# Kernel optimization log

Measured on AMD Instinct MI355X. Metric: run time of the kernel, lower is better.

The kernel has to match this reference:

```python
import jax, jax.numpy as jnp
import numpy as np

N = 100000      # nodes
E = 1600000     # edges
F = 64          # num_features
C = 10          # num_classes
L = 4           # num_layers
B = 128         # graphs in batch


def setup_inputs() -> dict:
    key = jax.random.key(0)
    ks = jax.random.split(key, 8)
    x = jax.random.normal(ks[0], (N, F), dtype=jnp.float32)
    edge_index = jax.random.randint(ks[1], (2, E), 0, N, dtype=jnp.int64)
    batch = jnp.sort(jax.random.randint(ks[2], (N,), 0, B, dtype=jnp.int64))
    scale = 1.0 / jnp.sqrt(jnp.float32(F))
    W1s = jax.random.normal(ks[3], (L, F, F), dtype=jnp.float32) * scale
    W2s = jax.random.normal(ks[4], (L, F, F), dtype=jnp.float32) * scale
    fc_w = jax.random.normal(ks[5], (C, F), dtype=jnp.float32) * scale
    fc_b = jax.random.normal(ks[6], (C,), dtype=jnp.float32) * 0.01
    return {"x": x, "edge_index": edge_index, "batch": batch,
            "W1s": W1s, "W2s": W2s, "fc_w": fc_w, "fc_b": fc_b}


def reference(x, edge_index, batch, W1s, W2s, fc_w, fc_b):
    src, dst = edge_index[0], edge_index[1]
    h = x
    for l in range(L):  # small fixed layer count
        # GINConv, eps=0: (1+eps)*x + sum of neighbor features (gather + scatter-add)
        agg = jax.ops.segment_sum(h[src], dst, num_segments=N)
        h = agg + h
        # MLP([F,F,F], bias=False, plain_last=False, act=sigmoid): two linears, each followed by sigmoid
        h = jax.nn.sigmoid(h @ W1s[l])
        h = jax.nn.sigmoid(h @ W2s[l])
    # global_add_pool over graphs in the batch
    xr = jax.ops.segment_sum(h, batch, num_segments=B)  # [B, F]
    logits = xr @ fc_w.T + fc_b                          # [B, C]
    return jax.nn.log_softmax(logits, axis=1), xr
```

## Files before the change

kernel.cpp:

```cpp
#include <hip/hip_runtime.h>
#include <hip/hip_bf16.h>

#define NN 100000
#define NE 1600000
#define FF 64
#define NC 10
#define NL 4
#define NB 128
#define LDST 72
#define CAP 48
#define NW 196
#define WCAPE 8704
#define PB_BIN 196
#define PB_XF 782
#define PB_W 32
#define PB_TOTAL (PB_BIN + PB_XF + PB_W + 1)

typedef __attribute__((ext_vector_type(8))) short short8;
typedef __attribute__((ext_vector_type(8))) unsigned short ushort8;
typedef __attribute__((ext_vector_type(4))) float f32x4;
typedef __attribute__((ext_vector_type(2))) float f32x2;

static __device__ __forceinline__ unsigned short f2bf(float x) {
  unsigned int u = __float_as_uint(x);
  unsigned int r = (u + 0x7fffu + ((u >> 16) & 1u)) >> 16;
  return (unsigned short)r;
}
static __device__ __forceinline__ float bf2f(unsigned short u) {
  return __uint_as_float(((unsigned int)u) << 16);
}
static __device__ __forceinline__ uint2 pack_f8(const float* a) {
  int w0 = __builtin_amdgcn_cvt_pk_fp8_f32(a[0], a[1], 0, false);
  w0 = __builtin_amdgcn_cvt_pk_fp8_f32(a[2], a[3], w0, true);
  int w1 = __builtin_amdgcn_cvt_pk_fp8_f32(a[4], a[5], 0, false);
  w1 = __builtin_amdgcn_cvt_pk_fp8_f32(a[6], a[7], w1, true);
  return make_uint2((unsigned)w0, (unsigned)w1);
}
static __device__ __forceinline__ void acc8w(f32x2* a, unsigned int x,
                                             unsigned int y) {
#if __has_builtin(__builtin_amdgcn_cvt_pk_f32_fp8)
  a[0] += __builtin_amdgcn_cvt_pk_f32_fp8((int)x, false);
  a[1] += __builtin_amdgcn_cvt_pk_f32_fp8((int)x, true);
  a[2] += __builtin_amdgcn_cvt_pk_f32_fp8((int)y, false);
  a[3] += __builtin_amdgcn_cvt_pk_f32_fp8((int)y, true);
#else
  a[0][0] += __builtin_amdgcn_cvt_f32_fp8((int)x, 0);
  a[0][1] += __builtin_amdgcn_cvt_f32_fp8((int)x, 1);
  a[1][0] += __builtin_amdgcn_cvt_f32_fp8((int)x, 2);
  a[1][1] += __builtin_amdgcn_cvt_f32_fp8((int)x, 3);
  a[2][0] += __builtin_amdgcn_cvt_f32_fp8((int)y, 0);
  a[2][1] += __builtin_amdgcn_cvt_f32_fp8((int)y, 1);
  a[3][0] += __builtin_amdgcn_cvt_f32_fp8((int)y, 2);
  a[3][1] += __builtin_amdgcn_cvt_f32_fp8((int)y, 3);
#endif
}
static __device__ __forceinline__ void acc16(f32x2* a, uint4 v) {
  acc8w(a, v.x, v.y);
  acc8w(a + 4, v.z, v.w);
}
static __device__ __forceinline__ unsigned char f2f8(float v) {
  return (unsigned char)(__builtin_amdgcn_cvt_pk_fp8_f32(v, v, 0, false) & 0xff);
}

__global__ __launch_bounds__(1024) void prepbin_kernel(
    const float* __restrict__ x, const int* __restrict__ src,
    const int* __restrict__ dst, const float* __restrict__ W1s,
    const float* __restrict__ W2s, uint2* __restrict__ xf8,
    unsigned short* __restrict__ Wt, int* __restrict__ wcnt,
    unsigned int* __restrict__ ebuf, uint2* __restrict__ hf8a,
    uint2* __restrict__ hf8b) {
  __shared__ int lcnt[NW];
  __shared__ int lbase[NW];
  int b = blockIdx.x;
  int t = threadIdx.x;
  if (b < PB_BIN) {
    int base = b * 8192 + t * 8;
    int d[8], s[8], wj[8];
    bool v[8];
    if (base + 8 <= NE) {
      *(int4*)(&d[0]) = *(const int4*)(dst + base);
      *(int4*)(&d[4]) = *(const int4*)(dst + base + 4);
      *(int4*)(&s[0]) = *(const int4*)(src + base);
      *(int4*)(&s[4]) = *(const int4*)(src + base + 4);
      #pragma unroll
      for (int j = 0; j < 8; ++j) v[j] = true;
    } else {
      #pragma unroll
      for (int j = 0; j < 8; ++j) {
        int e = base + j;
        v[j] = (e < NE);
        d[j] = v[j] ? dst[e] : 0;
        s[j] = v[j] ? src[e] : 0;
      }
    }
    #pragma unroll
    for (int j = 0; j < 8; ++j) wj[j] = d[j] >> 9;
    if (t < NW) lcnt[t] = 0;
    __syncthreads();
    #pragma unroll
    for (int j = 0; j < 8; ++j)
      if (v[j]) atomicAdd(&lcnt[wj[j]], 1);
    __syncthreads();
    if (t < NW) {
      lbase[t] = atomicAdd(&wcnt[t], lcnt[t]);
      lcnt[t] = 0;
    }
    __syncthreads();
    #pragma unroll
    for (int j = 0; j < 8; ++j) {
      if (v[j]) {
        int pos = lbase[wj[j]] + atomicAdd(&lcnt[wj[j]], 1);
        if (pos < WCAPE)
          ebuf[(size_t)wj[j] * WCAPE + pos] =
              ((unsigned)(d[j] & 511) << 17) | (unsigned)s[j];
      }
    }
  } else if (b < PB_BIN + PB_XF) {
    int g = (b - PB_BIN) * 1024 + t;
    if (g < NN * FF / 8) {
      size_t base = (size_t)g * 8;
      float4 a = *(const float4*)(x + base);
      float4 c = *(const float4*)(x + base + 4);
      float f[8] = {a.x, a.y, a.z, a.w, c.x, c.y, c.z, c.w};
      xf8[g] = pack_f8(f);
    }
  } else if (b < PB_BIN + PB_XF + PB_W) {
    int g = (b - PB_BIN - PB_XF) * 1024 + t;
    int mat = g >> 12, idx = g & 4095;
    int k = idx >> 6, n = idx & 63;
    int l = mat >> 1;
    const float* W = (mat & 1) ? (W2s + (size_t)l * FF * FF) : (W1s + (size_t)l * FF * FF);
    Wt[(size_t)mat * FF * FF + n * FF + k] = f2bf(W[k * FF + n]);
  } else {
    if (t < 8) {
      xf8[(size_t)NN * 8 + t] = make_uint2(0, 0);
      hf8a[(size_t)NN * 8 + t] = make_uint2(0, 0);
      hf8b[(size_t)NN * 8 + t] = make_uint2(0, 0);
    }
  }
}

__global__ __launch_bounds__(1024) void fillC_kernel(const unsigned int* __restrict__ ebuf,
                                                     const int* __restrict__ wcnt,
                                                     int* __restrict__ csr,
                                                     int* __restrict__ deg) {
  __shared__ int cur[512];
  int b = blockIdx.x;
  int t = threadIdx.x;
  int n0 = b << 9;
  if (t < 512) cur[t] = 0;
  __syncthreads();
  int cnt = min(wcnt[b], WCAPE);
  const unsigned int* ep = ebuf + (size_t)b * WCAPE;
  for (int i = t; i < cnt; i += 1024) {
    unsigned int e = ep[i];
    int dl = e >> 17;
    int s = (int)(e & 0x1ffffu);
    int slot = atomicAdd(&cur[dl], 1);
    if (slot < CAP) csr[(n0 + dl) * CAP + slot] = s;
  }
  __syncthreads();
  if (t < 512) {
    int node = n0 + t;
    if (node < NN) {
      int c = min(cur[t], CAP);
      deg[node] = c;
      int end = (c + 3) & ~3;
      for (; c < end; ++c) csr[node * CAP + c] = NN;
    }
  }
}

__global__ __launch_bounds__(256) void layer_kernel(
    const uint2* __restrict__ hin8, const int* __restrict__ csr,
    const int* __restrict__ deg, const unsigned short* __restrict__ Wt,
    uint2* __restrict__ hout8, const int* __restrict__ batch,
    float* __restrict__ xr, int last) {
  __shared__ __align__(16) unsigned short uL[64 * LDST];
  __shared__ __align__(16) unsigned char fb[64 * 64];
  int t = threadIdx.x;
  int row0 = blockIdx.x * 64;
  int lane = t & 63, w = t >> 6;
  int j2 = lane & 3;
  int gnode = lane >> 2;

  {
    int r = w * 16 + gnode;
    int node = row0 + r;
    f32x2 a[8] = {{0.f,0.f},{0.f,0.f},{0.f,0.f},{0.f,0.f},
                  {0.f,0.f},{0.f,0.f},{0.f,0.f},{0.f,0.f}};
    const uint4* hp4 = (const uint4*)hin8 + j2;
    if (node < NN) {
      acc16(a, hp4[(size_t)node * 4]);
      int i = node * CAP;
      int dg = deg[node];
      int endp = i + ((dg + 3) & ~3);
      for (; i < endp; i += 4) {
        int4 x0 = *(const int4*)(csr + i);
        uint4 r0 = hp4[(size_t)x0.x * 4];
        uint4 r1 = hp4[(size_t)x0.y * 4];
        uint4 r2 = hp4[(size_t)x0.z * 4];
        uint4 r3 = hp4[(size_t)x0.w * 4];
        acc16(a, r0); acc16(a, r1); acc16(a, r2); acc16(a, r3);
      }
    }
    ushort8 u0, u1;
    #pragma unroll
    for (int kk = 0; kk < 8; ++kk) u0[kk] = f2bf(a[kk >> 1][kk & 1]);
    #pragma unroll
    for (int kk = 0; kk < 8; ++kk) u1[kk] = f2bf(a[4 + (kk >> 1)][kk & 1]);
    *(ushort8*)(&uL[r * LDST + j2 * 16]) = u0;
    *(ushort8*)(&uL[r * LDST + j2 * 16 + 8]) = u1;
  }

  __builtin_amdgcn_sched_barrier(0);

  int m = lane & 15, q = lane >> 4;
  short8 b1[4][2], b2[4][2];
  #pragma unroll
  for (int c4 = 0; c4 < 4; ++c4) {
    #pragma unroll
    for (int s = 0; s < 2; ++s) {
      b1[c4][s] = *(const short8*)(Wt + (c4 * 16 + m) * FF + s * 32 + q * 8);
      b2[c4][s] = *(const short8*)(Wt + FF * FF + (c4 * 16 + m) * FF + s * 32 + q * 8);
    }
  }

  f32x4 acc[4] = {{0,0,0,0},{0,0,0,0},{0,0,0,0},{0,0,0,0}};
  #pragma unroll
  for (int s = 0; s < 2; ++s) {
    short8 a = *(const short8*)(&uL[(w * 16 + m) * LDST + s * 32 + q * 8]);
    #pragma unroll
    for (int c4 = 0; c4 < 4; ++c4)
      acc[c4] = __builtin_amdgcn_mfma_f32_16x16x32_bf16(a, b1[c4][s], acc[c4], 0, 0, 0);
  }
  #pragma unroll
  for (int c4 = 0; c4 < 4; ++c4) {
    #pragma unroll
    for (int i = 0; i < 4; ++i) {
      int r = w * 16 + q * 4 + i;
      float sgv = 1.f / (1.f + __expf(-acc[c4][i]));
      uL[r * LDST + c4 * 16 + m] = f2bf(sgv);
    }
  }

  f32x4 acc2[4] = {{0,0,0,0},{0,0,0,0},{0,0,0,0},{0,0,0,0}};
  #pragma unroll
  for (int s = 0; s < 2; ++s) {
    short8 a = *(const short8*)(&uL[(w * 16 + m) * LDST + s * 32 + q * 8]);
    #pragma unroll
    for (int c4 = 0; c4 < 4; ++c4)
      acc2[c4] = __builtin_amdgcn_mfma_f32_16x16x32_bf16(a, b2[c4][s], acc2[c4], 0, 0, 0);
  }
  if (last) {
    #pragma unroll
    for (int c4 = 0; c4 < 4; ++c4) {
      #pragma unroll
      for (int i = 0; i < 4; ++i) {
        int r = w * 16 + q * 4 + i;
        float sgv = 1.f / (1.f + __expf(-acc2[c4][i]));
        uL[r * LDST + c4 * 16 + m] = f2bf(sgv);
      }
    }
    int r0 = w * 16;
    int node0 = row0 + r0;
    if (node0 < NN) {
      float pacc = 0.f;
      int cur = batch[node0];
      #pragma unroll
      for (int r = 0; r < 16; ++r) {
        int node = node0 + r;
        if (node < NN) {
          int bb = batch[node];
          if (bb != cur) {
            unsafeAtomicAdd(&xr[(size_t)cur * FF + lane], pacc);
            pacc = 0.f; cur = bb;
          }
          pacc += bf2f(uL[(r0 + r) * LDST + lane]);
        }
      }
      unsafeAtomicAdd(&xr[(size_t)cur * FF + lane], pacc);
    }
  } else {
    #pragma unroll
    for (int c4 = 0; c4 < 4; ++c4) {
      #pragma unroll
      for (int i = 0; i < 4; ++i) {
        int r = w * 16 + q * 4 + i;
        float sgv = 1.f / (1.f + __expf(-acc2[c4][i]));
        fb[r * 64 + c4 * 16 + m] = f2f8(sgv);
      }
    }
    {
      int r = w * 16 + gnode;
      int node = row0 + r;
      if (node < NN) {
        uint4 v = *(const uint4*)(fb + r * 64 + j2 * 16);
        uint4* hout4 = (uint4*)hout8;
        hout4[(size_t)node * 4 + j2] = v;
      }
    }
  }
}

__global__ __launch_bounds__(64) void head_kernel(
    const float* __restrict__ xr, const float* __restrict__ fcw,
    const float* __restrict__ fcb, float* __restrict__ out) {
  int b = blockIdx.x, lane = threadIdx.x;
  float v = xr[(size_t)b * FF + lane];
  out[NB * NC + (size_t)b * FF + lane] = v;
  float logit[NC];
  #pragma unroll
  for (int c = 0; c < NC; ++c) {
    float s = v * fcw[c * FF + lane];
    #pragma unroll
    for (int o = 32; o > 0; o >>= 1) s += __shfl_xor(s, o, 64);
    logit[c] = s + fcb[c];
  }
  float mx = logit[0];
  #pragma unroll
  for (int c = 1; c < NC; ++c) mx = fmaxf(mx, logit[c]);
  float se = 0.f;
  #pragma unroll
  for (int c = 0; c < NC; ++c) se += expf(logit[c] - mx);
  float lse = logf(se);
  if (lane < NC) out[b * NC + lane] = logit[lane] - mx - lse;
}

extern "C" void kernel_launch(void* const* d_in, const int* in_sizes, int n_in,
                              void* d_out, int out_size, void* d_ws, size_t ws_size,
                              hipStream_t stream) {
  const float* x     = (const float*)d_in[0];
  const int*   ei    = (const int*)d_in[1];
  const int*   batch = (const int*)d_in[2];
  const float* W1s   = (const float*)d_in[3];
  const float* W2s   = (const float*)d_in[4];
  const float* fcw   = (const float*)d_in[5];
  const float* fcb   = (const float*)d_in[6];
  float* out = (float*)d_out;

  char* p = (char*)d_ws;
  uint2* xf8  = (uint2*)p; p += (size_t)(NN + 1) * 8 * 8;
  uint2* hf8a = (uint2*)p; p += (size_t)(NN + 1) * 8 * 8;
  uint2* hf8b = (uint2*)p; p += (size_t)(NN + 1) * 8 * 8;
  int* csr    = (int*)p;   p += (size_t)NN * CAP * 4;
  unsigned int* ebuf = (unsigned int*)p; p += (size_t)NW * WCAPE * 4;
  int* deg    = (int*)p;   p += (size_t)NN * 4;
  int* wcnt   = (int*)p;   p += (size_t)((NW + 63) & ~63) * 4;
  float* xr   = (float*)p; p += (size_t)NB * FF * 4;
  unsigned short* Wtall = (unsigned short*)p; p += (size_t)2 * NL * FF * FF * 2;

  const int* src = ei;
  const int* dst = ei + NE;

  hipMemsetAsync(wcnt, 0,
                 (size_t)((NW + 63) & ~63) * 4 + (size_t)NB * FF * 4, stream);

  prepbin_kernel<<<PB_TOTAL, 1024, 0, stream>>>(
      x, src, dst, W1s, W2s, xf8, Wtall, wcnt, ebuf, hf8a, hf8b);

  fillC_kernel<<<NW, 1024, 0, stream>>>(ebuf, wcnt, csr, deg);

  int layer_blocks = (NN + 63) / 64;
  const uint2* chain_in[NL]  = {xf8, hf8a, hf8b, hf8a};
  uint2*       chain_out[NL] = {hf8a, hf8b, hf8a, hf8b};
  for (int l = 0; l < NL; ++l) {
    int last = (l == NL - 1) ? 1 : 0;
    layer_kernel<<<layer_blocks, 256, 0, stream>>>(chain_in[l], csr, deg,
        Wtall + (size_t)l * 2 * FF * FF, chain_out[l], batch, xr, last);
  }

  head_kernel<<<NB, 64, 0, stream>>>(xr, fcw, fcb, out);
}
```

Measured before the change: 266.1 us.

## Split layer into aggregation and GEMM kernels with half-feature XCC-partitioned node tables

The fused layer kernel becomes two kernels. A gather/aggregation kernel reads node features from one of two 32-byte half-feature tables, chosen by the XCC id the block runs on, so each die's L2 caches only half of the feature table. A separate GEMM kernel reads the bf16 aggregates and runs the MLP. The aim is better cache locality for the random neighbour gathers, at the cost of an extra bf16 intermediate round trip through memory, an extra launch per layer, and atomic work-stealing counters.

```diff
diff --git a/kernel.cpp b/kernel.cpp
--- a/kernel.cpp
+++ b/kernel.cpp
@@ -15,11 +15,16 @@
 #define PB_XF 782
 #define PB_W 32
 #define PB_TOTAL (PB_BIN + PB_XF + PB_W + 1)
+#define HALF_TOTAL ((size_t)(NN + 1) * 32)
+#define NGA 782
+#define GEMM_BLOCKS ((NN + 63) / 64)
 
 typedef __attribute__((ext_vector_type(8))) short short8;
 typedef __attribute__((ext_vector_type(8))) unsigned short ushort8;
 typedef __attribute__((ext_vector_type(4))) float f32x4;
 typedef __attribute__((ext_vector_type(2))) float f32x2;
+typedef __attribute__((ext_vector_type(4))) int int4v;
+typedef __attribute__((ext_vector_type(4))) unsigned int uint4v;
 
 static __device__ __forceinline__ unsigned short f2bf(float x) {
   unsigned int u = __float_as_uint(x);
@@ -54,9 +59,9 @@
   a[3][1] += __builtin_amdgcn_cvt_f32_fp8((int)y, 3);
 #endif
 }
-static __device__ __forceinline__ void acc16(f32x2* a, uint4 v) {
-  acc8w(a, v.x, v.y);
-  acc8w(a + 4, v.z, v.w);
+static __device__ __forceinline__ void acc16v(f32x2* a, uint4v v) {
+  acc8w(a, v[0], v[1]);
+  acc8w(a + 4, v[2], v[3]);
 }
 static __device__ __forceinline__ unsigned char f2f8(float v) {
   return (unsigned char)(__builtin_amdgcn_cvt_pk_fp8_f32(v, v, 0, false) & 0xff);
@@ -65,10 +70,10 @@
 __global__ __launch_bounds__(1024) void prepbin_kernel(
     const float* __restrict__ x, const int* __restrict__ src,
     const int* __restrict__ dst, const float* __restrict__ W1s,
-    const float* __restrict__ W2s, uint2* __restrict__ xf8,
+    const float* __restrict__ W2s, unsigned char* __restrict__ Tx,
     unsigned short* __restrict__ Wt, int* __restrict__ wcnt,
-    unsigned int* __restrict__ ebuf, uint2* __restrict__ hf8a,
-    uint2* __restrict__ hf8b) {
+    unsigned int* __restrict__ ebuf, unsigned char* __restrict__ Ta,
+    unsigned char* __restrict__ Tb) {
   __shared__ int lcnt[NW];
   __shared__ int lbase[NW];
   int b = blockIdx.x;
@@ -117,12 +122,16 @@
     }
   } else if (b < PB_BIN + PB_XF) {
     int g = (b - PB_BIN) * 1024 + t;
-    if (g < NN * FF / 8) {
+    if (g < NN * 8) {
       size_t base = (size_t)g * 8;
       float4 a = *(const float4*)(x + base);
       float4 c = *(const float4*)(x + base + 4);
       float f[8] = {a.x, a.y, a.z, a.w, c.x, c.y, c.z, c.w};
-      xf8[g] = pack_f8(f);
+      uint2 pk = pack_f8(f);
+      int node = g >> 3, o = g & 7;
+      unsigned char* dstp = Tx + (size_t)(o >> 2) * HALF_TOTAL +
+                            (size_t)node * 32 + (o & 3) * 8;
+      *(uint2*)dstp = pk;
     }
   } else if (b < PB_BIN + PB_XF + PB_W) {
     int g = (b - PB_BIN - PB_XF) * 1024 + t;
@@ -132,10 +141,11 @@
     const float* W = (mat & 1) ? (W2s + (size_t)l * FF * FF) : (W1s + (size_t)l * FF * FF);
     Wt[(size_t)mat * FF * FF + n * FF + k] = f2bf(W[k * FF + n]);
   } else {
-    if (t < 8) {
-      xf8[(size_t)NN * 8 + t] = make_uint2(0, 0);
-      hf8a[(size_t)NN * 8 + t] = make_uint2(0, 0);
-      hf8b[(size_t)NN * 8 + t] = make_uint2(0, 0);
+    if (t < 24) {
+      int ti = t >> 3, h = (t >> 2) & 1, wd = t & 3;
+      unsigned char* tb = (ti == 0) ? Tx : (ti == 1) ? Ta : Tb;
+      *(uint2*)(tb + (size_t)h * HALF_TOTAL + (size_t)NN * 32 + wd * 8) =
+          make_uint2(0, 0);
     }
   }
 }
@@ -171,46 +181,71 @@
   }
 }
 
-__global__ __launch_bounds__(256) void layer_kernel(
-    const uint2* __restrict__ hin8, const int* __restrict__ csr,
-    const int* __restrict__ deg, const unsigned short* __restrict__ Wt,
-    uint2* __restrict__ hout8, const int* __restrict__ batch,
+__global__ __launch_bounds__(256) void agg_kernel(
+    const unsigned char* __restrict__ Tin, const int* __restrict__ csr,
+    const int* __restrict__ deg, unsigned short* __restrict__ agg,
+    int* __restrict__ ctr) {
+  __shared__ int sgf;
+  int t = threadIdx.x;
+  if (t == 0) {
+    unsigned xcc = __builtin_amdgcn_s_getreg((3 << 11) | 20) & 7;
+    int f = (xcc >= 4) ? 1 : 0;
+    int g = atomicAdd(&ctr[f], 1);
+    if (g >= NGA) { f = 1 - f; g = atomicAdd(&ctr[f], 1); }
+    sgf = (g << 1) | f;
+  }
+  __syncthreads();
+  int g = sgf >> 1, f = sgf & 1;
+  if (g >= NGA) return;
+  int lane = t & 63, w = t >> 6;
+  int j = lane & 1;
+  int node = g * 128 + w * 32 + (lane >> 1);
+  if (node >= NN) return;
+  f32x2 a[8] = {{0.f,0.f},{0.f,0.f},{0.f,0.f},{0.f,0.f},
+                {0.f,0.f},{0.f,0.f},{0.f,0.f},{0.f,0.f}};
+  const uint4v* hp = (const uint4v*)(Tin + (size_t)f * HALF_TOTAL) + j;
+  acc16v(a, hp[(size_t)node * 2]);
+  int i = node * CAP;
+  int endp = i + ((deg[node] + 3) & ~3);
+  for (; i < endp; i += 4) {
+    int4v x0 = __builtin_nontemporal_load((const int4v*)(csr + i));
+    uint4v r0 = hp[(size_t)x0[0] * 2];
+    uint4v r1 = hp[(size_t)x0[1] * 2];
+    uint4v r2 = hp[(size_t)x0[2] * 2];
+    uint4v r3 = hp[(size_t)x0[3] * 2];
+    acc16v(a, r0); acc16v(a, r1); acc16v(a, r2); acc16v(a, r3);
+  }
+  ushort8 u0, u1;
+  #pragma unroll
+  for (int kk = 0; kk < 8; ++kk) u0[kk] = f2bf(a[kk >> 1][kk & 1]);
+  #pragma unroll
+  for (int kk = 0; kk < 8; ++kk) u1[kk] = f2bf(a[4 + (kk >> 1)][kk & 1]);
+  unsigned short* dst = agg + (size_t)node * 64 + f * 32 + j * 16;
+  __builtin_nontemporal_store(u0, (ushort8*)dst);
+  __builtin_nontemporal_store(u1, (ushort8*)(dst + 8));
+}
+
+__global__ __launch_bounds__(256) void gemm_kernel(
+    const unsigned short* __restrict__ agg, const unsigned short* __restrict__ Wt,
+    unsigned char* __restrict__ Tout, const int* __restrict__ batch,
     float* __restrict__ xr, int last) {
   __shared__ __align__(16) unsigned short uL[64 * LDST];
   __shared__ __align__(16) unsigned char fb[64 * 64];
   int t = threadIdx.x;
   int row0 = blockIdx.x * 64;
   int lane = t & 63, w = t >> 6;
-  int j2 = lane & 3;
-  int gnode = lane >> 2;
 
   {
-    int r = w * 16 + gnode;
+    int r = w * 16 + (lane >> 2);
     int node = row0 + r;
-    f32x2 a[8] = {{0.f,0.f},{0.f,0.f},{0.f,0.f},{0.f,0.f},
-                  {0.f,0.f},{0.f,0.f},{0.f,0.f},{0.f,0.f}};
-    const uint4* hp4 = (const uint4*)hin8 + j2;
+    int qt = lane & 3;
     if (node < NN) {
-      acc16(a, hp4[(size_t)node * 4]);
-      int i = node * CAP;
-      int dg = deg[node];
-      int endp = i + ((dg + 3) & ~3);
-      for (; i < endp; i += 4) {
-        int4 x0 = *(const int4*)(csr + i);
-        uint4 r0 = hp4[(size_t)x0.x * 4];
-        uint4 r1 = hp4[(size_t)x0.y * 4];
-        uint4 r2 = hp4[(size_t)x0.z * 4];
-        uint4 r3 = hp4[(size_t)x0.w * 4];
-        acc16(a, r0); acc16(a, r1); acc16(a, r2); acc16(a, r3);
-      }
-    }
-    ushort8 u0, u1;
-    #pragma unroll
-    for (int kk = 0; kk < 8; ++kk) u0[kk] = f2bf(a[kk >> 1][kk & 1]);
-    #pragma unroll
-    for (int kk = 0; kk < 8; ++kk) u1[kk] = f2bf(a[4 + (kk >> 1)][kk & 1]);
-    *(ushort8*)(&uL[r * LDST + j2 * 16]) = u0;
-    *(ushort8*)(&uL[r * LDST + j2 * 16 + 8]) = u1;
+      const ushort8* srcp = (const ushort8*)(agg + (size_t)node * 64) + qt * 2;
+      ushort8 a0 = __builtin_nontemporal_load(srcp);
+      ushort8 a1 = __builtin_nontemporal_load(srcp + 1);
+      *(ushort8*)(&uL[r * LDST + qt * 16]) = a0;
+      *(ushort8*)(&uL[r * LDST + qt * 16 + 8]) = a1;
+    }
   }
 
   __builtin_amdgcn_sched_barrier(0);
@@ -292,12 +327,14 @@
       }
     }
     {
-      int r = w * 16 + gnode;
+      int r = w * 16 + (lane >> 2);
       int node = row0 + r;
+      int qt = lane & 3;
       if (node < NN) {
-        uint4 v = *(const uint4*)(fb + r * 64 + j2 * 16);
-        uint4* hout4 = (uint4*)hout8;
-        hout4[(size_t)node * 4 + j2] = v;
+        uint4 v = *(const uint4*)(fb + r * 64 + qt * 16);
+        unsigned char* dstp = Tout + (size_t)(qt >> 1) * HALF_TOTAL +
+                              (size_t)node * 32 + (qt & 1) * 16;
+        *(uint4*)dstp = v;
       }
     }
   }
@@ -340,33 +377,38 @@
   float* out = (float*)d_out;
 
   char* p = (char*)d_ws;
-  uint2* xf8  = (uint2*)p; p += (size_t)(NN + 1) * 8 * 8;
-  uint2* hf8a = (uint2*)p; p += (size_t)(NN + 1) * 8 * 8;
-  uint2* hf8b = (uint2*)p; p += (size_t)(NN + 1) * 8 * 8;
+  unsigned char* Tx = (unsigned char*)p; p += 2 * HALF_TOTAL;
+  unsigned char* Ta = (unsigned char*)p; p += 2 * HALF_TOTAL;
+  unsigned char* Tb = (unsigned char*)p; p += 2 * HALF_TOTAL;
   int* csr    = (int*)p;   p += (size_t)NN * CAP * 4;
-  unsigned int* ebuf = (unsigned int*)p; p += (size_t)NW * WCAPE * 4;
+  char* aggeb = p; p += (size_t)NN * FF * 2;
+  unsigned int* ebuf = (unsigned int*)aggeb;
+  unsigned short* agg = (unsigned short*)aggeb;
   int* deg    = (int*)p;   p += (size_t)NN * 4;
   int* wcnt   = (int*)p;   p += (size_t)((NW + 63) & ~63) * 4;
   float* xr   = (float*)p; p += (size_t)NB * FF * 4;
+  int* ctrs   = (int*)p;   p += 64;
   unsigned short* Wtall = (unsigned short*)p; p += (size_t)2 * NL * FF * FF * 2;
 
   const int* src = ei;
   const int* dst = ei + NE;
 
   hipMemsetAsync(wcnt, 0,
-                 (size_t)((NW + 63) & ~63) * 4 + (size_t)NB * FF * 4, stream);
+                 (size_t)((NW + 63) & ~63) * 4 + (size_t)NB * FF * 4 + 64,
+                 stream);
 
   prepbin_kernel<<<PB_TOTAL, 1024, 0, stream>>>(
-      x, src, dst, W1s, W2s, xf8, Wtall, wcnt, ebuf, hf8a, hf8b);
+      x, src, dst, W1s, W2s, Tx, Wtall, wcnt, ebuf, Ta, Tb);
 
   fillC_kernel<<<NW, 1024, 0, stream>>>(ebuf, wcnt, csr, deg);
 
-  int layer_blocks = (NN + 63) / 64;
-  const uint2* chain_in[NL]  = {xf8, hf8a, hf8b, hf8a};
-  uint2*       chain_out[NL] = {hf8a, hf8b, hf8a, hf8b};
+  const unsigned char* chain_in[NL]  = {Tx, Ta, Tb, Ta};
+  unsigned char*       chain_out[NL] = {Ta, Tb, Ta, Tb};
   for (int l = 0; l < NL; ++l) {
     int last = (l == NL - 1) ? 1 : 0;
-    layer_kernel<<<layer_blocks, 256, 0, stream>>>(chain_in[l], csr, deg,
+    agg_kernel<<<2 * NGA, 256, 0, stream>>>(chain_in[l], csr, deg, agg,
+                                            ctrs + l * 2);
+    gemm_kernel<<<GEMM_BLOCKS, 256, 0, stream>>>(agg,
         Wtall + (size_t)l * 2 * FF * FF, chain_out[l], batch, xr, last);
   }
 
```

Measured after the change: 419.0 us. 57.4% more time.
